# Kernel tuning notes

Measured on AMD Instinct MI355X. Metric: run time of the kernel, lower is better.

## Reference

```python
import jax, jax.numpy as jnp
import numpy as np

B = 65536
N_SPARSE = 20
N_VARLEN = 3
SEQ_LEN = 50
VOCAB = 100000
N_DENSE = 13


def setup_inputs() -> dict:
    key = jax.random.key(0)
    k1, k2, k3, k4, k5, k6 = jax.random.split(key, 6)
    sparse_ids = jax.random.randint(k1, (B, N_SPARSE), 0, VOCAB, dtype=jnp.int64 if jax.config.jax_enable_x64 else jnp.int32)
    varlen_ids = jax.random.randint(k2, (B, N_VARLEN, SEQ_LEN), 0, VOCAB, dtype=sparse_ids.dtype)
    dense_x = jax.random.normal(k3, (B, N_DENSE), dtype=jnp.float32)
    # dim-1 embedding table per feature, stacked: [n_feat, vocab]
    sparse_tables = jax.random.normal(k4, (N_SPARSE, VOCAB), dtype=jnp.float32)
    varlen_tables = jax.random.normal(k5, (N_VARLEN, VOCAB), dtype=jnp.float32)
    dense_w = jax.random.normal(k6, (N_DENSE,), dtype=jnp.float32) * 1e-4
    return {
        "sparse_ids": sparse_ids,
        "varlen_ids": varlen_ids,
        "dense_x": dense_x,
        "sparse_tables": sparse_tables,
        "varlen_tables": varlen_tables,
        "dense_w": dense_w,
    }


def reference(sparse_ids, varlen_ids, dense_x, sparse_tables, varlen_tables, dense_w):
    # per-feature dim-1 embedding gather for single-value sparse feats: [B, Fs]
    fs = jnp.arange(N_SPARSE)
    sparse_vals = sparse_tables[fs[None, :], sparse_ids]
    # varlen gather: [B, Fv, L]; mask_zero=True -> id 0 contributes nothing; sum pooling
    fv = jnp.arange(N_VARLEN)
    varlen_vals = varlen_tables[fv[None, :, None], varlen_ids]
    mask = (varlen_ids != 0).astype(varlen_vals.dtype)
    varlen_pool = jnp.sum(varlen_vals * mask, axis=-1)  # [B, Fv]
    # reduce_sum over concat([sparse_vals, varlen_pool]) == sum of both sums
    logit = jnp.sum(sparse_vals, axis=-1) + jnp.sum(varlen_pool, axis=-1)
    # linear dense logit: concat(dense) @ W[:,1], squeezed
    logit = logit + dense_x @ dense_w
    return logit  # [B]
```

## Files before the change

### kernel.cpp

```cpp
#include <hip/hip_runtime.h>

constexpr int B        = 65536;
constexpr int N_SPARSE = 20;
constexpr int N_VARLEN = 3;
constexpr int SEQ_LEN  = 50;
constexpr int VOCAB    = 100000;
constexpr int N_DENSE  = 13;
constexpr int VAR_TOT  = N_VARLEN * SEQ_LEN;

__global__ __launch_bounds__(256) void logit_kernel(
    const int*   __restrict__ sparse_ids,
    const int*   __restrict__ varlen_ids,
    const float* __restrict__ dense_x,
    const float* __restrict__ sparse_tables,
    const float* __restrict__ varlen_tables,
    const float* __restrict__ dense_w,
    float*       __restrict__ out)
{
    const int tid = blockIdx.x * blockDim.x + threadIdx.x;
    const int g   = tid >> 4;
    const int t   = tid & 15;

    const int4*   vptr = (const int4*)(varlen_ids) + (long)g * 75;
    const int4*   sptr = (const int4*)(sparse_ids) + (long)g * 10;
    const float2* dptr = (const float2*)(dense_x)  + (long)g * 13;

    int4 vid[5];
    #pragma unroll
    for (int k = 0; k < 4; ++k) vid[k] = vptr[t + 16 * k];
    const bool v5 = (t + 64) < 75;
    if (v5) vid[4] = vptr[t + 64];

    int4 sid;
    const bool hs = (t < 10);
    if (hs) sid = sptr[t];

    float2 dx;
    const bool hd = (t < 13);
    if (hd) dx = dptr[t];

    float acc0 = 0.f, acc1 = 0.f;

    #pragma unroll
    for (int k = 0; k < 5; ++k) {
        if (k == 4 && !v5) continue;
        const int s0 = 4 * (t + 16 * k);
        const int ids[4] = { vid[k].x, vid[k].y, vid[k].z, vid[k].w };
        #pragma unroll
        for (int j = 0; j < 4; ++j) {
            const int s  = s0 + j;
            const bool r1 = (s >= VAR_TOT);
            const int p  = r1 ? (s - VAR_TOT) : s;
            const int v  = (p >= 100) ? 2 : (p >= 50 ? 1 : 0);
            const float val = varlen_tables[v * VOCAB + ids[j]];
            const float m   = (ids[j] != 0) ? val : 0.f;
            acc0 += r1 ? 0.f : m;
            acc1 += r1 ? m   : 0.f;
        }
    }

    if (hs) {
        const int s0 = 4 * t;
        const int ids[4] = { sid.x, sid.y, sid.z, sid.w };
        #pragma unroll
        for (int j = 0; j < 4; ++j) {
            const int s  = s0 + j;
            const bool r1 = (s >= N_SPARSE);
            const int f  = r1 ? (s - N_SPARSE) : s;
            const float val = sparse_tables[f * VOCAB + ids[j]];
            acc0 += r1 ? 0.f : val;
            acc1 += r1 ? val : 0.f;
        }
    }

    if (hd) {
        const int s0 = 2 * t;
        {
            const int s = s0;
            const bool r1 = (s >= N_DENSE);
            const int d = r1 ? (s - N_DENSE) : s;
            const float prod = dx.x * dense_w[d];
            acc0 += r1 ? 0.f : prod;
            acc1 += r1 ? prod : 0.f;
        }
        {
            const int s = s0 + 1;
            const bool r1 = (s >= N_DENSE);
            const int d = r1 ? (s - N_DENSE) : s;
            const float prod = dx.y * dense_w[d];
            acc0 += r1 ? 0.f : prod;
            acc1 += r1 ? prod : 0.f;
        }
    }

    #pragma unroll
    for (int o = 1; o < 16; o <<= 1) {
        acc0 += __shfl_xor(acc0, o);
        acc1 += __shfl_xor(acc1, o);
    }
    if (t == 0) ((float2*)out)[g] = make_float2(acc0, acc1);
}

extern "C" void kernel_launch(void* const* d_in, const int* in_sizes, int n_in,
                              void* d_out, int out_size, void* d_ws, size_t ws_size,
                              hipStream_t stream) {
    const int*   sparse_ids    = (const int*)d_in[0];
    const int*   varlen_ids    = (const int*)d_in[1];
    const float* dense_x       = (const float*)d_in[2];
    const float* sparse_tables = (const float*)d_in[3];
    const float* varlen_tables = (const float*)d_in[4];
    const float* dense_w       = (const float*)d_in[5];
    float*       out           = (float*)d_out;

    const int threads = 256;
    const int total   = (B / 2) * 16;
    const int blocks  = total / threads;
    logit_kernel<<<blocks, threads, 0, stream>>>(
        sparse_ids, varlen_ids, dense_x, sparse_tables, varlen_tables, dense_w, out);
}
```

Measured before the change: 136.9 us.

## Split dense dot into separate kernel and gather sparse/varlen via atomics

Moves the dense dot product into its own kernel that initializes the output. The gather kernel then gives varlen and sparse lookups separate block ranges. Each range accumulates into the output with atomicAdd, so every block does uniform work instead of mixing all three streams in a 16-lane group. This adds a second launch and per-row atomics. Sparse rows are now read one row per thread with strided int4 loads, which coalesce worse.

```diff
diff --git a/kernel.cpp b/kernel.cpp
--- a/kernel.cpp
+++ b/kernel.cpp
@@ -8,97 +8,93 @@
 constexpr int N_DENSE  = 13;
 constexpr int VAR_TOT  = N_VARLEN * SEQ_LEN;
 
-__global__ __launch_bounds__(256) void logit_kernel(
-    const int*   __restrict__ sparse_ids,
-    const int*   __restrict__ varlen_ids,
+constexpr int NB_VAR    = (B / 2) * 16 / 256;
+constexpr int NB_SPARSE = B / 256;
+
+__global__ __launch_bounds__(256) void dense_kernel(
     const float* __restrict__ dense_x,
-    const float* __restrict__ sparse_tables,
-    const float* __restrict__ varlen_tables,
     const float* __restrict__ dense_w,
     float*       __restrict__ out)
 {
-    const int tid = blockIdx.x * blockDim.x + threadIdx.x;
-    const int g   = tid >> 4;
-    const int t   = tid & 15;
+    const int row = blockIdx.x * blockDim.x + threadIdx.x;
+    if (row >= B) return;
+    const float* drow = dense_x + (long)row * N_DENSE;
+    float acc = 0.f;
+    #pragma unroll
+    for (int d = 0; d < N_DENSE; ++d) acc += drow[d] * dense_w[d];
+    out[row] = acc;
+}
 
-    const int4*   vptr = (const int4*)(varlen_ids) + (long)g * 75;
-    const int4*   sptr = (const int4*)(sparse_ids) + (long)g * 10;
-    const float2* dptr = (const float2*)(dense_x)  + (long)g * 13;
+__global__ __launch_bounds__(256) void gather_kernel(
+    const int*   __restrict__ sparse_ids,
+    const int*   __restrict__ varlen_ids,
+    const float* __restrict__ sparse_tables,
+    const float* __restrict__ varlen_tables,
+    float*       __restrict__ out)
+{
+    if (blockIdx.x < NB_VAR) {
+        const int tid = blockIdx.x * blockDim.x + threadIdx.x;
+        const int g   = tid >> 4;
+        const int t   = tid & 15;
 
-    int4 vid[5];
-    #pragma unroll
-    for (int k = 0; k < 4; ++k) vid[k] = vptr[t + 16 * k];
-    const bool v5 = (t + 64) < 75;
-    if (v5) vid[4] = vptr[t + 64];
+        const int4* vptr = (const int4*)(varlen_ids) + (long)g * 75;
 
-    int4 sid;
-    const bool hs = (t < 10);
-    if (hs) sid = sptr[t];
+        int4 vid[5];
+        #pragma unroll
+        for (int k = 0; k < 4; ++k) vid[k] = vptr[t + 16 * k];
+        const bool v5 = (t + 64) < 75;
+        if (v5) vid[4] = vptr[t + 64];
 
-    float2 dx;
-    const bool hd = (t < 13);
-    if (hd) dx = dptr[t];
+        float acc0 = 0.f, acc1 = 0.f;
 
-    float acc0 = 0.f, acc1 = 0.f;
+        #pragma unroll
+        for (int k = 0; k < 5; ++k) {
+            if (k == 4 && !v5) continue;
+            const int s0 = 4 * (t + 16 * k);
+            const int ids[4] = { vid[k].x, vid[k].y, vid[k].z, vid[k].w };
+            #pragma unroll
+            for (int j = 0; j < 4; ++j) {
+                const int s  = s0 + j;
+                const bool r1 = (s >= VAR_TOT);
+                const int p  = r1 ? (s - VAR_TOT) : s;
+                const int v  = (p >= 100) ? 2 : (p >= 50 ? 1 : 0);
+                const float val = varlen_tables[v * VOCAB + ids[j]];
+                const float m   = (ids[j] != 0) ? val : 0.f;
+                acc0 += r1 ? 0.f : m;
+                acc1 += r1 ? m   : 0.f;
+            }
+        }
 
-    #pragma unroll
-    for (int k = 0; k < 5; ++k) {
-        if (k == 4 && !v5) continue;
-        const int s0 = 4 * (t + 16 * k);
-        const int ids[4] = { vid[k].x, vid[k].y, vid[k].z, vid[k].w };
         #pragma unroll
-        for (int j = 0; j < 4; ++j) {
-            const int s  = s0 + j;
-            const bool r1 = (s >= VAR_TOT);
-            const int p  = r1 ? (s - VAR_TOT) : s;
-            const int v  = (p >= 100) ? 2 : (p >= 50 ? 1 : 0);
-            const float val = varlen_tables[v * VOCAB + ids[j]];
-            const float m   = (ids[j] != 0) ? val : 0.f;
-            acc0 += r1 ? 0.f : m;
-            acc1 += r1 ? m   : 0.f;
+        for (int o = 1; o < 16; o <<= 1) {
+            acc0 += __shfl_xor(acc0, o);
+            acc1 += __shfl_xor(acc1, o);
         }
+        if (t == 0) {
+            atomicAdd(out + 2 * g,     acc0);
+            atomicAdd(out + 2 * g + 1, acc1);
+        }
+    } else {
+        const int row = (blockIdx.x - NB_VAR) * blockDim.x + threadIdx.x;
+        if (row >= B) return;
+
+        const int4* sptr = (const int4*)(sparse_ids) + (long)row * 5;
+        int4 sid[5];
+        #pragma unroll
+        for (int k = 0; k < 5; ++k) sid[k] = sptr[k];
+
+        float acc = 0.f;
+        #pragma unroll
+        for (int k = 0; k < 5; ++k) {
+            const int ids[4] = { sid[k].x, sid[k].y, sid[k].z, sid[k].w };
+            #pragma unroll
+            for (int j = 0; j < 4; ++j) {
+                const int f = 4 * k + j;
+                acc += sparse_tables[f * VOCAB + ids[j]];
+            }
+        }
+        atomicAdd(out + row, acc);
     }
-
-    if (hs) {
-        const int s0 = 4 * t;
-        const int ids[4] = { sid.x, sid.y, sid.z, sid.w };
-        #pragma unroll
-        for (int j = 0; j < 4; ++j) {
-            const int s  = s0 + j;
-            const bool r1 = (s >= N_SPARSE);
-            const int f  = r1 ? (s - N_SPARSE) : s;
-            const float val = sparse_tables[f * VOCAB + ids[j]];
-            acc0 += r1 ? 0.f : val;
-            acc1 += r1 ? val : 0.f;
-        }
-    }
-
-    if (hd) {
-        const int s0 = 2 * t;
-        {
-            const int s = s0;
-            const bool r1 = (s >= N_DENSE);
-            const int d = r1 ? (s - N_DENSE) : s;
-            const float prod = dx.x * dense_w[d];
-            acc0 += r1 ? 0.f : prod;
-            acc1 += r1 ? prod : 0.f;
-        }
-        {
-            const int s = s0 + 1;
-            const bool r1 = (s >= N_DENSE);
-            const int d = r1 ? (s - N_DENSE) : s;
-            const float prod = dx.y * dense_w[d];
-            acc0 += r1 ? 0.f : prod;
-            acc1 += r1 ? prod : 0.f;
-        }
-    }
-
-    #pragma unroll
-    for (int o = 1; o < 16; o <<= 1) {
-        acc0 += __shfl_xor(acc0, o);
-        acc1 += __shfl_xor(acc1, o);
-    }
-    if (t == 0) ((float2*)out)[g] = make_float2(acc0, acc1);
 }
 
 extern "C" void kernel_launch(void* const* d_in, const int* in_sizes, int n_in,
@@ -112,9 +108,7 @@
     const float* dense_w       = (const float*)d_in[5];
     float*       out           = (float*)d_out;
 
-    const int threads = 256;
-    const int total   = (B / 2) * 16;
-    const int blocks  = total / threads;
-    logit_kernel<<<blocks, threads, 0, stream>>>(
-        sparse_ids, varlen_ids, dense_x, sparse_tables, varlen_tables, dense_w, out);
+    dense_kernel<<<B / 256, 256, 0, stream>>>(dense_x, dense_w, out);
+    gather_kernel<<<NB_VAR + NB_SPARSE, 256, 0, stream>>>(
+        sparse_ids, varlen_ids, sparse_tables, varlen_tables, out);
 }
```

New measurement: 136.8 us. No clear change (-0.1%).
